# Performance work log

Measured on AMD Instinct MI355X. Metric: run time of the kernel, lower is better.

Reference implementation:

```python
import jax, jax.numpy as jnp
import numpy as np

N = 512    # nnodes
H = 8      # attention heads
C = 32     # gnn_repr_size (per head)
ER = 32    # edge_repr_size
FE = 3     # feat_emb_size
E = 16384  # edges (avg degree 32)


def gat_conv(x, edge_index, edge_attr, W, att_src, att_dst, We, att_edge, b):
    """PyG GATConv (edge_dim=1, concat=True, add_self_loops=True, eval mode)."""
    n = x.shape[0]
    h_, c_ = att_src.shape
    row, col = edge_index[0], edge_index[1]
    # self loops with fill_value='mean': mean of incoming edge_attr per target node
    deg = jax.ops.segment_sum(jnp.ones_like(edge_attr), col, num_segments=n)
    loop_attr = jax.ops.segment_sum(edge_attr, col, num_segments=n) / jnp.maximum(deg, 1.0)
    ar = jnp.arange(n)
    row = jnp.concatenate([row, ar])
    col = jnp.concatenate([col, ar])
    ea = jnp.concatenate([edge_attr, loop_attr])
    # node projections [n, H, C]
    h = (x @ W.T).reshape(n, h_, c_)
    a_src = jnp.sum(h * att_src, axis=-1)  # [n, H]
    a_dst = jnp.sum(h * att_dst, axis=-1)  # [n, H]
    e = (ea[:, None] @ We.T).reshape(-1, h_, c_)  # [E', H, C]
    a_e = jnp.sum(e * att_edge, axis=-1)          # [E', H]
    alpha = jax.nn.leaky_relu(a_src[row] + a_dst[col] + a_e, 0.2)
    # softmax over edges grouped by destination node
    amax = jax.ops.segment_max(alpha, col, num_segments=n)
    ex = jnp.exp(alpha - amax[col])
    denom = jax.ops.segment_sum(ex, col, num_segments=n)
    alpha = ex / (denom[col] + 1e-16)
    out = jax.ops.segment_sum(h[row] * alpha[..., None], col, num_segments=n)
    return out.reshape(n, h_ * c_) + b


def setup_inputs():
    key = jax.random.key(0)
    ks = jax.random.split(key, 24)
    s = 0.05
    HC = H * C
    in_len = N * ER + 3 * N + 3 * FE  # combiner1 input length
    return {
        "dist": jax.random.uniform(ks[0], (N, N), dtype=jnp.float32),
        "markov": jax.random.uniform(ks[1], (N, N), dtype=jnp.float32),
        "demand": jax.random.normal(ks[2], (N,), dtype=jnp.float32),
        "W_week": jax.random.normal(ks[3], (7, FE)) * s,
        "W_cap": jax.random.normal(ks[4], (26, FE)) * s,
        "W_veh": jax.random.normal(ks[5], (15, FE)) * s,
        "g1_W": jax.random.normal(ks[6], (HC, 1)) * s,
        "g1_att_src": jax.random.normal(ks[7], (H, C)) * s,
        "g1_att_dst": jax.random.normal(ks[8], (H, C)) * s,
        "g1_We": jax.random.normal(ks[9], (HC, 1)) * s,
        "g1_att_edge": jax.random.normal(ks[10], (H, C)) * s,
        "g1_b": jnp.zeros((HC,), dtype=jnp.float32),
        "g2_W": jax.random.normal(ks[11], (HC, HC)) * s,
        "g2_att_src": jax.random.normal(ks[12], (H, C)) * s,
        "g2_att_dst": jax.random.normal(ks[13], (H, C)) * s,
        "g2_We": jax.random.normal(ks[14], (HC, 1)) * s,
        "g2_att_edge": jax.random.normal(ks[15], (H, C)) * s,
        "g2_b": jnp.zeros((HC,), dtype=jnp.float32),
        "Wes": jax.random.normal(ks[16], (ER, 2 * HC)) * s,
        "bes": jnp.zeros((ER,), dtype=jnp.float32),
        "Wc1": jax.random.normal(ks[17], (N, in_len)) * 0.01,
        "bc1": jnp.zeros((N,), dtype=jnp.float32),
        "Wc2": jax.random.normal(ks[18], (N, N)) * s,
        "bc2": jnp.zeros((N,), dtype=jnp.float32),
        "stops": jax.random.randint(ks[19], (256,), 0, N),
        "edge_index": jax.random.randint(ks[20], (2, E), 0, N),
        "weekday": 3,
        "vehicles": 7,
        "capacity": 12,
    }


def reference(dist, markov, demand, W_week, W_cap, W_veh,
              g1_W, g1_att_src, g1_att_dst, g1_We, g1_att_edge, g1_b,
              g2_W, g2_att_src, g2_att_dst, g2_We, g2_att_edge, g2_b,
              Wes, bes, Wc1, bc1, Wc2, bc2,
              stops, edge_index, weekday, vehicles, capacity):
    n = dist.shape[0]
    dist = (dist - dist.min()) / (dist.max() - dist.min())
    x = demand[:, None]  # [n, 1]
    ea = markov[edge_index[0], edge_index[1]]  # [E]
    x = jax.nn.relu(gat_conv(x, edge_index, ea, g1_W, g1_att_src, g1_att_dst, g1_We, g1_att_edge, g1_b))
    x = jax.nn.relu(gat_conv(x, edge_index, ea, g2_W, g2_att_src, g2_att_dst, g2_We, g2_att_edge, g2_b))
    HC_ = x.shape[1]
    # all-pairs edge representation: concat(x[i], x[j]) over meshgrid -> [n*n, 2*HC]
    er = jnp.concatenate([
        jnp.broadcast_to(x[:, None, :], (n, n, HC_)),
        jnp.broadcast_to(x[None, :, :], (n, n, HC_)),
    ], axis=-1).reshape(n * n, 2 * HC_)
    er = (er @ Wes.T + bes).reshape(n, -1)  # [n, n*ER]
    week = jnp.broadcast_to(W_week[weekday], (n, W_week.shape[1]))
    cap = jnp.broadcast_to(W_cap[capacity], (n, W_cap.shape[1]))
    veh = jnp.broadcast_to(W_veh[vehicles], (n, W_veh.shape[1]))
    stop = jnp.broadcast_to(jnp.zeros((n,), dtype=dist.dtype).at[stops].set(1.0)[None, :], (n, n))
    feat = jnp.concatenate([er, dist, markov, week, cap, veh, stop], axis=1)
    out = jax.nn.relu(feat @ Wc1.T + bc1) @ Wc2.T + bc2
    return out
```

## Files before the change

### kernel.cpp

```cpp
#include <hip/hip_runtime.h>
#include <hip/hip_bf16.h>

typedef __hip_bfloat16 bf16;
typedef __attribute__((ext_vector_type(8))) short bf16x8;
typedef __attribute__((ext_vector_type(4))) float f32x4;

#define NNODE 512
#define NEDGE 16384
#define INLEN 17929
#define K1    1056

#define WS_EA      0
#define WS_CSRC    16384
#define WS_CEA     32768
#define WS_DEG     49152
#define WS_STARTS  49664
#define WS_LATTR   50176
#define WS_MM      50688
#define WS_MMP     50690
#define WS_STOPV   50818
#define WS_AE      51330
#define WS_PS      51346
#define WS_H       55552
#define WS_G2WT    186624
#define WS_H2      317696
#define WS_ASRC    448768
#define WS_ADST    452864
#define WS_UV      456960
#define WS_K       489728
#define WS_APACK   490240
#define WS_BPACK   760576
#define WS_OUT1    1030912
#define WS_WC2B    1161984
#define WS_WESF    1293056
#define WS_ASRC2   1309440
#define WS_ADST2   1313536
#define WS_CURSOR  1317632
#define WS_DEGP    1318144
#define WS_LSUMP   1350912

__global__ __launch_bounds__(256)
void k_prep(const float* __restrict__ demand, const float* __restrict__ W1,
            const float* __restrict__ att_s, const float* __restrict__ att_d,
            const int* __restrict__ stops, const float* __restrict__ Wes,
            const float* __restrict__ dist, const float* __restrict__ markov,
            const int* __restrict__ eidx,
            const float* __restrict__ g1We, const float* __restrict__ g1ae,
            const float* __restrict__ g2We, const float* __restrict__ g2ae,
            const float* __restrict__ g2W,  const float* __restrict__ g2as,
            const float* __restrict__ g2ad, float* ws){
  int b = blockIdx.x, tid = threadIdx.x;
  if (b < 512){
    int hd = tid>>5, c = tid&31;
    float hv = demand[b] * W1[tid];
    ws[WS_H + b*256 + tid] = hv;
    float ps = hv * att_s[tid];
    float pd = hv * att_d[tid];
    for (int off=16; off; off>>=1){ ps += __shfl_down(ps,off,32); pd += __shfl_down(pd,off,32); }
    if (c==0){ ws[WS_ASRC + b*8+hd]=ps; ws[WS_ADST + b*8+hd]=pd; }
  } else if (b == 512){
    ws[WS_STOPV+tid] = 0.f; ws[WS_STOPV+256+tid] = 0.f;
    __syncthreads();
    ws[WS_STOPV + stops[tid]] = 1.0f;
    if (tid < 8){
      float s=0.f; for (int c=0;c<32;c++) s += g1We[tid*32+c]*g1ae[tid*32+c];
      ws[WS_AE+tid]=s;
    } else if (tid < 16){
      int h=tid-8; float s=0.f; for (int c=0;c<32;c++) s += g2We[h*32+c]*g2ae[h*32+c];
      ws[WS_AE+8+h]=s;
    }
  } else if (b < 515){
    for (int idx = (b-513)*8192 + tid; idx < (b-512)*8192; idx += 256){
      int k = idx>>8, c = idx&255;
      ws[WS_WESF+idx] = (k<32) ? Wes[k*512+c] : Wes[(k-32)*512+256+c];
    }
  } else if (b < 579){
    __shared__ float smn[256], smx[256];
    int p = b-515;
    float mn = 3.4e38f, mx = -3.4e38f;
    for (int k=0;k<16;k++){
      float v = dist[p*4096 + k*256 + tid];
      mn = fminf(mn,v); mx = fmaxf(mx,v);
    }
    smn[tid]=mn; smx[tid]=mx; __syncthreads();
    for (int off=128; off; off>>=1){
      if (tid<off){ smn[tid]=fminf(smn[tid],smn[tid+off]); smx[tid]=fmaxf(smx[tid],smx[tid+off]); }
      __syncthreads();
    }
    if (tid==0){ ws[WS_MMP+p]=smn[0]; ws[WS_MMP+64+p]=smx[0]; }
  } else if (b < 643){
    __shared__ int   hd_[512];
    __shared__ float hf_[512];
    int k = b-579;
    hd_[tid]=0; hd_[256+tid]=0; hf_[tid]=0.f; hf_[256+tid]=0.f;
    __syncthreads();
    int e = k*256 + tid;
    int r = eidx[e], c = eidx[NEDGE+e];
    float a = markov[r*NNODE + c];
    ws[WS_EA+e] = a;
    atomicAdd(&hd_[c], 1);
    atomicAdd(&hf_[c], a);
    __syncthreads();
    ((int*)(ws+WS_DEGP))[k*512+tid]     = hd_[tid];
    ((int*)(ws+WS_DEGP))[k*512+256+tid] = hd_[256+tid];
    ws[WS_LSUMP + k*512+tid]     = hf_[tid];
    ws[WS_LSUMP + k*512+256+tid] = hf_[256+tid];
  } else if (b < 659){
    int j = b-643;
    const float* att = (j<8) ? g2as : g2ad;
    int h = j&7;
    float s = 0.f;
    for (int c=0;c<32;c++) s += att[h*32+c] * g2W[(h*32+c)*256 + tid];
    ws[WS_PS + j*256 + tid] = s;
  } else if (b < 675){
    __shared__ float T[64][65];
    int tb = b-659, tr = tb>>2, tc = tb&3;
    int w = tid>>6, c = tid&63;
    for (int k=0;k<16;k++){
      int r = k*4 + w;
      T[r][c] = g2W[(tr*64+r)*256 + tc*64 + c];
    }
    __syncthreads();
    for (int k=0;k<16;k++){
      int r = k*4 + w;
      ws[WS_G2WT + (tc*64+r)*256 + tr*64 + c] = T[c][r];
    }
  } else {
    ((int*)(ws+WS_CURSOR))[tid] = 0;
    ((int*)(ws+WS_CURSOR))[256+tid] = 0;
  }
}

__global__ __launch_bounds__(512)
void k_scansc(const int* __restrict__ eidx, float* ws){
  __shared__ int sc[512];
  __shared__ int startS[512];
  __shared__ float rmn[64], rmx[64];
  int t = threadIdx.x, b = blockIdx.x;
  const int* dp = (const int*)(ws+WS_DEGP);
  int d = 0;
  for (int k=0;k<64;k++) d += dp[k*512+t];
  sc[t] = d; __syncthreads();
  for (int off=1; off<512; off<<=1){
    int v = (t>=off) ? sc[t-off] : 0; __syncthreads();
    sc[t] += v; __syncthreads();
  }
  startS[t] = sc[t]-d;
  if (b == 0){
    float l = 0.f;
    for (int k=0;k<64;k++) l += ws[WS_LSUMP+k*512+t];
    ((int*)(ws+WS_STARTS))[t] = startS[t];
    ((int*)(ws+WS_DEG))[t] = d;
    ws[WS_LATTR+t] = l / (float)(d>1 ? d : 1);
    if (t < 64){ rmn[t]=ws[WS_MMP+t]; rmx[t]=ws[WS_MMP+64+t]; }
    __syncthreads();
    if (t == 0){
      float mn=rmn[0], mx=rmx[0];
      for (int i=1;i<64;i++){ mn=fminf(mn,rmn[i]); mx=fmaxf(mx,rmx[i]); }
      ws[WS_MM]=mn; ws[WS_MM+1]=mx;
    }
  }
  __syncthreads();
  int e = b*512 + t;
  int c = eidx[NEDGE+e];
  int p = startS[c] + atomicAdd((int*)(ws+WS_CURSOR)+c, 1);
  ((int*)(ws+WS_CSRC))[p] = eidx[e];
  ws[WS_CEA+p] = ws[WS_EA+e];
}

template<int MODE>
__global__ __launch_bounds__(256)
void k_agg(const float* __restrict__ hbuf, const float* __restrict__ asrc,
           const float* __restrict__ adst, const int* __restrict__ csrc,
           const float* __restrict__ cea, const int* __restrict__ starts,
           const int* __restrict__ deg, const float* __restrict__ lattr,
           const float* __restrict__ AEp, const float* __restrict__ bvec,
           const float* __restrict__ dist, const float* __restrict__ markov,
           float* ws){
  int t = blockIdx.x, tid = threadIdx.x, hd = tid>>5;
  __shared__ float AE[8], m[8], den[8], alpha[8];
  __shared__ float L[32*8];
  __shared__ float xrow[256];
  __shared__ float uvrow[64];
  if (tid < 8) AE[tid] = AEp[tid];
  __syncthreads();
  int d = deg[t], s0 = starts[t];
  if (tid < 8){
    float aself = asrc[t*8+tid] + adst[t*8+tid] + lattr[t]*AE[tid];
    aself = aself>=0.f ? aself : 0.2f*aself;
    m[tid] = aself; den[tid] = 1.0f;
  }
  __syncthreads();
  float acc = hbuf[t*256+tid];
  int el = tid>>3, h2i = tid&7;
  float adt2 = adst[t*8+h2i], ae2 = AE[h2i];
  for (int e0=0; e0<d; e0+=32){
    int ce = d-e0 < 32 ? d-e0 : 32;
    float lg = -3.4e38f;
    if (el < ce){
      int src = csrc[s0+e0+el];
      float a = asrc[src*8+h2i] + adt2 + cea[s0+e0+el]*ae2;
      lg = a>=0.f ? a : 0.2f*a;
    }
    L[el*8+h2i] = lg;
    __syncthreads();
    if (tid < 8){
      float mm = m[tid];
      for (int e=0;e<ce;e++) mm = fmaxf(mm, L[e*8+tid]);
      float al = __expf(m[tid]-mm);
      float dd = den[tid]*al;
      for (int e=0;e<ce;e++) dd += __expf(L[e*8+tid]-mm);
      m[tid]=mm; den[tid]=dd; alpha[tid]=al;
    }
    __syncthreads();
    if (el < ce) L[el*8+h2i] = __expf(lg - m[h2i]);
    __syncthreads();
    acc *= alpha[hd];
    for (int e=0;e<ce;e++){
      int sre = csrc[s0+e0+e];
      acc += L[e*8+hd] * hbuf[sre*256+tid];
    }
    __syncthreads();
  }
  float v = fmaxf(acc/den[hd] + bvec[tid], 0.f);
  xrow[tid] = v;
  __syncthreads();
  if (MODE == 1){
    const float* g2wt = ws + WS_G2WT;
    float hr = 0.f;
    for (int c=0;c<256;c++) hr += xrow[c] * g2wt[c*256 + tid];
    ws[WS_H2 + t*256 + tid] = hr;
    if (tid < 64){
      int j = tid>>2, q = tid&3;
      const float* pr = ws + WS_PS + j*256 + q*64;
      const float* xr = xrow + q*64;
      float p = 0.f;
      for (int c=0;c<64;c++) p += xr[c]*pr[c];
      p += __shfl_down(p,2,4);
      p += __shfl_down(p,1,4);
      if (q==0){
        if (j<8) ws[WS_ASRC2 + t*8+j] = p;
        else     ws[WS_ADST2 + t*8+(j-8)] = p;
      }
    }
  } else {
    int k = tid>>2, q = tid&3;
    const float* wr = ws + WS_WESF + k*256 + q*64;
    const float* xr = xrow + q*64;
    float p = 0.f;
    for (int c=0;c<64;c++) p += xr[c]*wr[c];
    p += __shfl_down(p,2,4);
    p += __shfl_down(p,1,4);
    if (q==0){ ws[WS_UV + t*64+k] = p; uvrow[k] = p; }
    __syncthreads();
    float mn = ws[WS_MM], mx = ws[WS_MM+1];
    float inv = 1.0f/(mx-mn);
    bf16* ap = (bf16*)(ws+WS_APACK);
    for (int j=tid; j<K1; j+=256){
      float v2;
      if (j<32)       v2 = uvrow[j];
      else if (j<544) v2 = (dist[t*512 + j-32] - mn) * inv;
      else            v2 = markov[t*512 + j-544];
      ap[(size_t)t*K1 + j] = __float2bfloat16(v2);
    }
  }
}

__global__ __launch_bounds__(1024)
void k_skpack(const float* __restrict__ Wc1, const float* __restrict__ bc1,
              const float* __restrict__ bes, const float* __restrict__ Wweek,
              const float* __restrict__ Wcap, const float* __restrict__ Wveh,
              const int* __restrict__ wd, const int* __restrict__ vh,
              const int* __restrict__ cp, const float* __restrict__ Wc2,
              float* ws){
  int o = blockIdx.x, tid = threadIdx.x;
  __shared__ float besf[32];
  __shared__ float red[1024];
  if (tid<32) besf[tid] = bes[tid];
  __syncthreads();
  const float* wr = Wc1 + (size_t)o*INLEN;
  bf16* bp  = (bf16*)(ws+WS_BPACK);
  bf16* w2b = (bf16*)(ws+WS_WC2B);
  float be = besf[tid&31];
  const float* uvp = ws + WS_UV + ((tid>>5)<<6) + 32 + (tid&31);
  float sP = 0.f, tP0=0.f, tP1=0.f, tP2=0.f, tP3=0.f;
  #pragma unroll
  for (int i=0;i<16;i+=4){
    float w0 = wr[tid + 1024*(i+0)];
    float w1 = wr[tid + 1024*(i+1)];
    float w2 = wr[tid + 1024*(i+2)];
    float w3 = wr[tid + 1024*(i+3)];
    float u0 = uvp[2048*(i+0)];
    float u1 = uvp[2048*(i+1)];
    float u2 = uvp[2048*(i+2)];
    float u3 = uvp[2048*(i+3)];
    sP += (w0+w1)+(w2+w3);
    tP0 += w0*(u0+be);
    tP1 += w1*(u1+be);
    tP2 += w2*(u2+be);
    tP3 += w3*(u3+be);
  }
  float tP = (tP0+tP1)+(tP2+tP3);
  if (tid < 512) tP += ws[WS_STOPV+tid] * wr[17417+tid];
  if (tid < 9){
    int g = tid/3, f = tid-g*3;
    float sv = (g==0) ? Wweek[wd[0]*3+f]
             : (g==1) ? Wcap[cp[0]*3+f]
                      : Wveh[vh[0]*3+f];
    tP += sv * wr[17408+tid];
  }
  red[tid] = sP; __syncthreads();
  for (int off=512; off>=32; off>>=1){
    if (tid<off) red[tid] += red[tid+off];
    __syncthreads();
  }
  if (tid<32) bp[(size_t)o*K1 + tid] = __float2bfloat16(red[tid]);
  __syncthreads();
  red[tid] = tP; __syncthreads();
  for (int off=512; off; off>>=1){
    if (tid<off) red[tid] += red[tid+off];
    __syncthreads();
  }
  if (tid==0) ws[WS_K+o] = red[0] + bc1[o];
  bp[(size_t)o*K1 + 32 + tid] = __float2bfloat16(wr[16384+tid]);
  if (tid < 512) w2b[o*512+tid] = __float2bfloat16(Wc2[o*512+tid]);
}

template<bool RELU, bool BF16OUT>
__global__ __launch_bounds__(256)
void gemm_mfma(const bf16* __restrict__ A, const bf16* __restrict__ B,
               const float* __restrict__ bias, float* __restrict__ Cf,
               bf16* __restrict__ Cb, int M, int N, int K){
  __shared__ short Als[2048];
  __shared__ short Bls[2048];
  const int tid = threadIdx.x;
  const int bm = blockIdx.y*64, bn = blockIdx.x*64;
  const int wave = tid>>6, lane = tid&63;
  const int wm = wave>>1, wn = wave&1;
  const int r = lane&15, q = lane>>4;
  f32x4 acc[2][2] = {};
  const int lrow = tid>>2, lq = tid&3;
  const bf16* Ag = A + (size_t)(bm+lrow)*K + lq*8;
  const bf16* Bg = B + (size_t)(bn+lrow)*K + lq*8;
  const int sidx = (lq*64+lrow)*8;
  for (int k0=0; k0<K; k0+=32){
    float4 av = *(const float4*)(Ag + k0);
    float4 bv = *(const float4*)(Bg + k0);
    *(float4*)(&Als[sidx]) = av;
    *(float4*)(&Bls[sidx]) = bv;
    __syncthreads();
    #pragma unroll
    for (int i=0;i<2;i++){
      bf16x8 af = *(const bf16x8*)(&Als[(q*64 + wm*32 + i*16 + r)*8]);
      #pragma unroll
      for (int j=0;j<2;j++){
        bf16x8 bfr = *(const bf16x8*)(&Bls[(q*64 + wn*32 + j*16 + r)*8]);
        acc[i][j] = __builtin_amdgcn_mfma_f32_16x16x32_bf16(af, bfr, acc[i][j], 0,0,0);
      }
    }
    __syncthreads();
  }
  #pragma unroll
  for (int i=0;i<2;i++){
    int row = bm + wm*32 + i*16 + q*4;
    #pragma unroll
    for (int j=0;j<2;j++){
      int col = bn + wn*32 + j*16 + r;
      float bi = bias ? bias[col] : 0.f;
      #pragma unroll
      for (int g=0; g<4; g++){
        float v = acc[i][j][g] + bi;
        if (RELU) v = fmaxf(v, 0.f);
        if (BF16OUT) Cb[(size_t)(row+g)*N + col] = __float2bfloat16(v);
        else         Cf[(size_t)(row+g)*N + col] = v;
      }
    }
  }
}

extern "C" void kernel_launch(void* const* d_in, const int* in_sizes, int n_in,
                              void* d_out, int out_size, void* d_ws, size_t ws_size,
                              hipStream_t stream){
  const float* dist   = (const float*)d_in[0];
  const float* markov = (const float*)d_in[1];
  const float* demand = (const float*)d_in[2];
  const float* Wweek  = (const float*)d_in[3];
  const float* Wcap   = (const float*)d_in[4];
  const float* Wveh   = (const float*)d_in[5];
  const float* g1W    = (const float*)d_in[6];
  const float* g1as   = (const float*)d_in[7];
  const float* g1ad   = (const float*)d_in[8];
  const float* g1We   = (const float*)d_in[9];
  const float* g1ae   = (const float*)d_in[10];
  const float* g1b    = (const float*)d_in[11];
  const float* g2W    = (const float*)d_in[12];
  const float* g2as   = (const float*)d_in[13];
  const float* g2ad   = (const float*)d_in[14];
  const float* g2We   = (const float*)d_in[15];
  const float* g2ae   = (const float*)d_in[16];
  const float* g2b    = (const float*)d_in[17];
  const float* Wes    = (const float*)d_in[18];
  const float* bes    = (const float*)d_in[19];
  const float* Wc1    = (const float*)d_in[20];
  const float* bc1    = (const float*)d_in[21];
  const float* Wc2    = (const float*)d_in[22];
  const float* bc2    = (const float*)d_in[23];
  const int*   stops  = (const int*)d_in[24];
  const int*   eidx   = (const int*)d_in[25];
  const int*   wd     = (const int*)d_in[26];
  const int*   vh     = (const int*)d_in[27];
  const int*   cp     = (const int*)d_in[28];
  float* out = (float*)d_out;
  float* ws = (float*)d_ws;

  const int*   csrc   = (const int*)(ws+WS_CSRC);
  const float* cea    = ws+WS_CEA;
  const int*   starts = (const int*)(ws+WS_STARTS);
  const int*   deg    = (const int*)(ws+WS_DEG);
  const float* lattr  = ws+WS_LATTR;

  k_prep<<<676,256,0,stream>>>(demand, g1W, g1as, g1ad, stops, Wes, dist, markov, eidx,
                               g1We, g1ae, g2We, g2ae, g2W, g2as, g2ad, ws);
  k_scansc<<<32,512,0,stream>>>(eidx, ws);
  k_agg<1><<<512,256,0,stream>>>(ws+WS_H, ws+WS_ASRC, ws+WS_ADST, csrc, cea, starts, deg,
                                 lattr, ws+WS_AE, g1b, dist, markov, ws);
  k_agg<2><<<512,256,0,stream>>>(ws+WS_H2, ws+WS_ASRC2, ws+WS_ADST2, csrc, cea, starts, deg,
                                 lattr, ws+WS_AE+8, g2b, dist, markov, ws);
  k_skpack<<<512,1024,0,stream>>>(Wc1, bc1, bes, Wweek, Wcap, Wveh, wd, vh, cp, Wc2, ws);
  gemm_mfma<true,true><<<dim3(8,8),256,0,stream>>>((const bf16*)(ws+WS_APACK), (const bf16*)(ws+WS_BPACK),
                                                   ws+WS_K, nullptr, (bf16*)(ws+WS_OUT1), 512, 512, K1);
  gemm_mfma<false,false><<<dim3(8,8),256,0,stream>>>((const bf16*)(ws+WS_OUT1), (const bf16*)(ws+WS_WC2B),
                                                     bc2, out, nullptr, 512, 512, 512);
}
```

Baseline: 212.8 us.

## Replace CSR build with per-node edge scan inside aggregation kernels

```diff
diff --git a/kernel.cpp b/kernel.cpp
--- a/kernel.cpp
+++ b/kernel.cpp
@@ -10,41 +10,30 @@
 #define INLEN 17929
 #define K1    1056
 
-#define WS_EA      0
-#define WS_CSRC    16384
-#define WS_CEA     32768
-#define WS_DEG     49152
-#define WS_STARTS  49664
-#define WS_LATTR   50176
-#define WS_MM      50688
-#define WS_MMP     50690
-#define WS_STOPV   50818
-#define WS_AE      51330
-#define WS_PS      51346
-#define WS_H       55552
-#define WS_G2WT    186624
-#define WS_H2      317696
-#define WS_ASRC    448768
-#define WS_ADST    452864
-#define WS_UV      456960
-#define WS_K       489728
-#define WS_APACK   490240
-#define WS_BPACK   760576
-#define WS_OUT1    1030912
-#define WS_WC2B    1161984
-#define WS_WESF    1293056
-#define WS_ASRC2   1309440
-#define WS_ADST2   1313536
-#define WS_CURSOR  1317632
-#define WS_DEGP    1318144
-#define WS_LSUMP   1350912
+#define WS_MMP     0
+#define WS_STOPV   128
+#define WS_AE      640
+#define WS_PS      656
+#define WS_H       5120
+#define WS_G2WT    136192
+#define WS_H2      201728
+#define WS_ASRC    332800
+#define WS_ADST    336896
+#define WS_UV      340992
+#define WS_K       373760
+#define WS_APACK   374272
+#define WS_BPACK   644608
+#define WS_OUT1    914944
+#define WS_WC2B    1046016
+#define WS_WESF    1177088
+#define WS_ASRC2   1193472
+#define WS_ADST2   1197568
 
 __global__ __launch_bounds__(256)
 void k_prep(const float* __restrict__ demand, const float* __restrict__ W1,
             const float* __restrict__ att_s, const float* __restrict__ att_d,
             const int* __restrict__ stops, const float* __restrict__ Wes,
-            const float* __restrict__ dist, const float* __restrict__ markov,
-            const int* __restrict__ eidx,
+            const float* __restrict__ dist,
             const float* __restrict__ g1We, const float* __restrict__ g1ae,
             const float* __restrict__ g2We, const float* __restrict__ g2ae,
             const float* __restrict__ g2W,  const float* __restrict__ g2as,
@@ -88,33 +77,16 @@
       __syncthreads();
     }
     if (tid==0){ ws[WS_MMP+p]=smn[0]; ws[WS_MMP+64+p]=smx[0]; }
-  } else if (b < 643){
-    __shared__ int   hd_[512];
-    __shared__ float hf_[512];
-    int k = b-579;
-    hd_[tid]=0; hd_[256+tid]=0; hf_[tid]=0.f; hf_[256+tid]=0.f;
-    __syncthreads();
-    int e = k*256 + tid;
-    int r = eidx[e], c = eidx[NEDGE+e];
-    float a = markov[r*NNODE + c];
-    ws[WS_EA+e] = a;
-    atomicAdd(&hd_[c], 1);
-    atomicAdd(&hf_[c], a);
-    __syncthreads();
-    ((int*)(ws+WS_DEGP))[k*512+tid]     = hd_[tid];
-    ((int*)(ws+WS_DEGP))[k*512+256+tid] = hd_[256+tid];
-    ws[WS_LSUMP + k*512+tid]     = hf_[tid];
-    ws[WS_LSUMP + k*512+256+tid] = hf_[256+tid];
-  } else if (b < 659){
-    int j = b-643;
+  } else if (b < 595){
+    int j = b-579;
     const float* att = (j<8) ? g2as : g2ad;
     int h = j&7;
     float s = 0.f;
     for (int c=0;c<32;c++) s += att[h*32+c] * g2W[(h*32+c)*256 + tid];
     ws[WS_PS + j*256 + tid] = s;
-  } else if (b < 675){
+  } else {
     __shared__ float T[64][65];
-    int tb = b-659, tr = tb>>2, tc = tb&3;
+    int tb = b-595, tr = tb>>2, tc = tb&3;
     int w = tid>>6, c = tid&63;
     for (int k=0;k<16;k++){
       int r = k*4 + w;
@@ -125,111 +97,96 @@
       int r = k*4 + w;
       ws[WS_G2WT + (tc*64+r)*256 + tr*64 + c] = T[c][r];
     }
-  } else {
-    ((int*)(ws+WS_CURSOR))[tid] = 0;
-    ((int*)(ws+WS_CURSOR))[256+tid] = 0;
-  }
-}
-
-__global__ __launch_bounds__(512)
-void k_scansc(const int* __restrict__ eidx, float* ws){
-  __shared__ int sc[512];
-  __shared__ int startS[512];
-  __shared__ float rmn[64], rmx[64];
-  int t = threadIdx.x, b = blockIdx.x;
-  const int* dp = (const int*)(ws+WS_DEGP);
-  int d = 0;
-  for (int k=0;k<64;k++) d += dp[k*512+t];
-  sc[t] = d; __syncthreads();
-  for (int off=1; off<512; off<<=1){
-    int v = (t>=off) ? sc[t-off] : 0; __syncthreads();
-    sc[t] += v; __syncthreads();
-  }
-  startS[t] = sc[t]-d;
-  if (b == 0){
-    float l = 0.f;
-    for (int k=0;k<64;k++) l += ws[WS_LSUMP+k*512+t];
-    ((int*)(ws+WS_STARTS))[t] = startS[t];
-    ((int*)(ws+WS_DEG))[t] = d;
-    ws[WS_LATTR+t] = l / (float)(d>1 ? d : 1);
-    if (t < 64){ rmn[t]=ws[WS_MMP+t]; rmx[t]=ws[WS_MMP+64+t]; }
-    __syncthreads();
-    if (t == 0){
-      float mn=rmn[0], mx=rmx[0];
-      for (int i=1;i<64;i++){ mn=fminf(mn,rmn[i]); mx=fmaxf(mx,rmx[i]); }
-      ws[WS_MM]=mn; ws[WS_MM+1]=mx;
-    }
-  }
-  __syncthreads();
-  int e = b*512 + t;
-  int c = eidx[NEDGE+e];
-  int p = startS[c] + atomicAdd((int*)(ws+WS_CURSOR)+c, 1);
-  ((int*)(ws+WS_CSRC))[p] = eidx[e];
-  ws[WS_CEA+p] = ws[WS_EA+e];
+  }
 }
 
 template<int MODE>
 __global__ __launch_bounds__(256)
 void k_agg(const float* __restrict__ hbuf, const float* __restrict__ asrc,
-           const float* __restrict__ adst, const int* __restrict__ csrc,
-           const float* __restrict__ cea, const int* __restrict__ starts,
-           const int* __restrict__ deg, const float* __restrict__ lattr,
-           const float* __restrict__ AEp, const float* __restrict__ bvec,
-           const float* __restrict__ dist, const float* __restrict__ markov,
+           const float* __restrict__ adst, const int* __restrict__ eidx,
+           const float* __restrict__ markov, const float* __restrict__ AEp,
+           const float* __restrict__ bvec, const float* __restrict__ dist,
            float* ws){
   int t = blockIdx.x, tid = threadIdx.x, hd = tid>>5;
-  __shared__ float AE[8], m[8], den[8], alpha[8];
-  __shared__ float L[32*8];
-  __shared__ float xrow[256];
-  __shared__ float uvrow[64];
-  if (tid < 8) AE[tid] = AEp[tid];
-  __syncthreads();
-  int d = deg[t], s0 = starts[t];
-  if (tid < 8){
-    float aself = asrc[t*8+tid] + adst[t*8+tid] + lattr[t]*AE[tid];
+  __shared__ int   srcE[256];
+  __shared__ float eaE[256];
+  __shared__ float Lall[256*8];
+  __shared__ float AE[8], mh[8], dh[8], sw[8];
+  __shared__ float xrow[256], uvrow[64];
+  __shared__ int   cnt;
+  __shared__ float easum;
+  __shared__ float mnS, mxS;
+  if (tid==0){ cnt=0; easum=0.f; }
+  if (tid<8) AE[tid]=AEp[tid];
+  __syncthreads();
+  for (int e0=0; e0<NEDGE; e0+=256){
+    int col = eidx[NEDGE+e0+tid];
+    if (col==t){
+      int p = atomicAdd(&cnt,1);
+      int row = eidx[e0+tid];
+      float a = markov[row*NNODE+t];
+      if (p<256){ srcE[p]=row; eaE[p]=a; }
+      atomicAdd(&easum, a);
+    }
+  }
+  __syncthreads();
+  int d = cnt<256 ? cnt : 256;
+  float lattr = easum / (float)(cnt>1 ? cnt : 1);
+  {
+    int h8 = tid&7, eq = tid>>3;
+    float adt = adst[t*8+h8], aeh = AE[h8];
+    for (int e = eq; e < d; e += 32){
+      int s = srcE[e];
+      float a = asrc[s*8+h8] + adt + eaE[e]*aeh;
+      Lall[e*8+h8] = a>=0.f ? a : 0.2f*a;
+    }
+  }
+  __syncthreads();
+  {
+    int h = tid>>5, j = tid&31;
+    float aself = asrc[t*8+h] + adst[t*8+h] + lattr*AE[h];
     aself = aself>=0.f ? aself : 0.2f*aself;
-    m[tid] = aself; den[tid] = 1.0f;
-  }
-  __syncthreads();
-  float acc = hbuf[t*256+tid];
-  int el = tid>>3, h2i = tid&7;
-  float adt2 = adst[t*8+h2i], ae2 = AE[h2i];
-  for (int e0=0; e0<d; e0+=32){
-    int ce = d-e0 < 32 ? d-e0 : 32;
-    float lg = -3.4e38f;
-    if (el < ce){
-      int src = csrc[s0+e0+el];
-      float a = asrc[src*8+h2i] + adt2 + cea[s0+e0+el]*ae2;
-      lg = a>=0.f ? a : 0.2f*a;
-    }
-    L[el*8+h2i] = lg;
-    __syncthreads();
-    if (tid < 8){
-      float mm = m[tid];
-      for (int e=0;e<ce;e++) mm = fmaxf(mm, L[e*8+tid]);
-      float al = __expf(m[tid]-mm);
-      float dd = den[tid]*al;
-      for (int e=0;e<ce;e++) dd += __expf(L[e*8+tid]-mm);
-      m[tid]=mm; den[tid]=dd; alpha[tid]=al;
-    }
-    __syncthreads();
-    if (el < ce) L[el*8+h2i] = __expf(lg - m[h2i]);
-    __syncthreads();
-    acc *= alpha[hd];
-    for (int e=0;e<ce;e++){
-      int sre = csrc[s0+e0+e];
-      acc += L[e*8+hd] * hbuf[sre*256+tid];
-    }
-    __syncthreads();
-  }
-  float v = fmaxf(acc/den[hd] + bvec[tid], 0.f);
+    float mm = aself;
+    for (int e=j; e<d; e+=32) mm = fmaxf(mm, Lall[e*8+h]);
+    for (int off=16; off; off>>=1) mm = fmaxf(mm, __shfl_down(mm,off,32));
+    mm = __shfl(mm, 0, 32);
+    float dd = 0.f;
+    for (int e=j; e<d; e+=32) dd += __expf(Lall[e*8+h]-mm);
+    for (int off=16; off; off>>=1) dd += __shfl_down(dd,off,32);
+    if (j==0){
+      float se = __expf(aself-mm);
+      mh[h]=mm; dh[h]=dd+se+1e-16f; sw[h]=se;
+    }
+  }
+  __syncthreads();
+  {
+    int h8 = tid&7;
+    for (int e = tid>>3; e < d; e += 32)
+      Lall[e*8+h8] = __expf(Lall[e*8+h8] - mh[h8]);
+  }
+  __syncthreads();
+  float a0 = sw[hd]*hbuf[t*256+tid], a1=0.f, a2=0.f, a3=0.f;
+  int e = 0;
+  for (; e+4<=d; e+=4){
+    a0 += Lall[(e+0)*8+hd]*hbuf[srcE[e+0]*256+tid];
+    a1 += Lall[(e+1)*8+hd]*hbuf[srcE[e+1]*256+tid];
+    a2 += Lall[(e+2)*8+hd]*hbuf[srcE[e+2]*256+tid];
+    a3 += Lall[(e+3)*8+hd]*hbuf[srcE[e+3]*256+tid];
+  }
+  for (; e<d; e++) a0 += Lall[e*8+hd]*hbuf[srcE[e]*256+tid];
+  float v = fmaxf(((a0+a1)+(a2+a3))/dh[hd] + bvec[tid], 0.f);
   xrow[tid] = v;
   __syncthreads();
   if (MODE == 1){
     const float* g2wt = ws + WS_G2WT;
-    float hr = 0.f;
-    for (int c=0;c<256;c++) hr += xrow[c] * g2wt[c*256 + tid];
-    ws[WS_H2 + t*256 + tid] = hr;
+    float h0=0.f,h1=0.f,h2=0.f,h3=0.f;
+    for (int c=0;c<256;c+=4){
+      h0 += xrow[c+0]*g2wt[(c+0)*256+tid];
+      h1 += xrow[c+1]*g2wt[(c+1)*256+tid];
+      h2 += xrow[c+2]*g2wt[(c+2)*256+tid];
+      h3 += xrow[c+3]*g2wt[(c+3)*256+tid];
+    }
+    ws[WS_H2 + t*256 + tid] = (h0+h1)+(h2+h3);
     if (tid < 64){
       int j = tid>>2, q = tid&3;
       const float* pr = ws + WS_PS + j*256 + q*64;
@@ -252,15 +209,23 @@
     p += __shfl_down(p,2,4);
     p += __shfl_down(p,1,4);
     if (q==0){ ws[WS_UV + t*64+k] = p; uvrow[k] = p; }
-    __syncthreads();
-    float mn = ws[WS_MM], mx = ws[WS_MM+1];
-    float inv = 1.0f/(mx-mn);
+    if (tid < 64){
+      float mn = ws[WS_MMP+tid], mx = ws[WS_MMP+64+tid];
+      for (int off=32; off; off>>=1){
+        mn = fminf(mn, __shfl_down(mn,off));
+        mx = fmaxf(mx, __shfl_down(mx,off));
+      }
+      if (tid==0){ mnS=mn; mxS=mx; }
+    }
+    __syncthreads();
+    float mn = mnS, inv = 1.0f/(mxS-mnS);
     bf16* ap = (bf16*)(ws+WS_APACK);
+    const float* mrow = markov + t*512;
     for (int j=tid; j<K1; j+=256){
       float v2;
       if (j<32)       v2 = uvrow[j];
       else if (j<544) v2 = (dist[t*512 + j-32] - mn) * inv;
-      else            v2 = markov[t*512 + j-544];
+      else            v2 = mrow[j-544];
       ap[(size_t)t*K1 + j] = __float2bfloat16(v2);
     }
   }
@@ -413,19 +378,12 @@
   float* out = (float*)d_out;
   float* ws = (float*)d_ws;
 
-  const int*   csrc   = (const int*)(ws+WS_CSRC);
-  const float* cea    = ws+WS_CEA;
-  const int*   starts = (const int*)(ws+WS_STARTS);
-  const int*   deg    = (const int*)(ws+WS_DEG);
-  const float* lattr  = ws+WS_LATTR;
-
-  k_prep<<<676,256,0,stream>>>(demand, g1W, g1as, g1ad, stops, Wes, dist, markov, eidx,
+  k_prep<<<611,256,0,stream>>>(demand, g1W, g1as, g1ad, stops, Wes, dist,
                                g1We, g1ae, g2We, g2ae, g2W, g2as, g2ad, ws);
-  k_scansc<<<32,512,0,stream>>>(eidx, ws);
-  k_agg<1><<<512,256,0,stream>>>(ws+WS_H, ws+WS_ASRC, ws+WS_ADST, csrc, cea, starts, deg,
-                                 lattr, ws+WS_AE, g1b, dist, markov, ws);
-  k_agg<2><<<512,256,0,stream>>>(ws+WS_H2, ws+WS_ASRC2, ws+WS_ADST2, csrc, cea, starts, deg,
-                                 lattr, ws+WS_AE+8, g2b, dist, markov, ws);
+  k_agg<1><<<512,256,0,stream>>>(ws+WS_H, ws+WS_ASRC, ws+WS_ADST, eidx, markov,
+                                 ws+WS_AE, g1b, dist, ws);
+  k_agg<2><<<512,256,0,stream>>>(ws+WS_H2, ws+WS_ASRC2, ws+WS_ADST2, eidx, markov,
+                                 ws+WS_AE+8, g2b, dist, ws);
   k_skpack<<<512,1024,0,stream>>>(Wc1, bc1, bes, Wweek, Wcap, Wveh, wd, vh, cp, Wc2, ws);
   gemm_mfma<true,true><<<dim3(8,8),256,0,stream>>>((const bf16*)(ws+WS_APACK), (const bf16*)(ws+WS_BPACK),
                                                    ws+WS_K, nullptr, (bf16*)(ws+WS_OUT1), 512, 512, K1);
```

Result: slower. 223.4 us (+5.0%).

## Replace online softmax in GAT aggregation with two-pass shared-memory softmax

Applied to the files above, without the earlier changes.

```diff
diff --git a/kernel.cpp b/kernel.cpp
--- a/kernel.cpp
+++ b/kernel.cpp
@@ -178,58 +178,71 @@
            const float* __restrict__ dist, const float* __restrict__ markov,
            float* ws){
   int t = blockIdx.x, tid = threadIdx.x, hd = tid>>5;
-  __shared__ float AE[8], m[8], den[8], alpha[8];
-  __shared__ float L[32*8];
-  __shared__ float xrow[256];
-  __shared__ float uvrow[64];
-  if (tid < 8) AE[tid] = AEp[tid];
+  __shared__ int   srcE[256];
+  __shared__ float eaE[256];
+  __shared__ float Lall[256*8];
+  __shared__ float AE[8], mh[8], dh[8], sw[8];
+  __shared__ float xrow[256], uvrow[64];
+  if (tid<8) AE[tid]=AEp[tid];
   __syncthreads();
   int d = deg[t], s0 = starts[t];
-  if (tid < 8){
-    float aself = asrc[t*8+tid] + adst[t*8+tid] + lattr[t]*AE[tid];
+  if (d > 256) d = 256;
+  for (int e=tid; e<d; e+=256){ srcE[e]=csrc[s0+e]; eaE[e]=cea[s0+e]; }
+  __syncthreads();
+  {
+    int h8 = tid&7;
+    float adt = adst[t*8+h8], aeh = AE[h8];
+    for (int e = tid>>3; e < d; e += 32){
+      float a = asrc[srcE[e]*8+h8] + adt + eaE[e]*aeh;
+      Lall[e*8+h8] = a>=0.f ? a : 0.2f*a;
+    }
+  }
+  __syncthreads();
+  {
+    int h = tid>>5, j = tid&31;
+    float aself = asrc[t*8+h] + adst[t*8+h] + lattr[t]*AE[h];
     aself = aself>=0.f ? aself : 0.2f*aself;
-    m[tid] = aself; den[tid] = 1.0f;
-  }
-  __syncthreads();
-  float acc = hbuf[t*256+tid];
-  int el = tid>>3, h2i = tid&7;
-  float adt2 = adst[t*8+h2i], ae2 = AE[h2i];
-  for (int e0=0; e0<d; e0+=32){
-    int ce = d-e0 < 32 ? d-e0 : 32;
-    float lg = -3.4e38f;
-    if (el < ce){
-      int src = csrc[s0+e0+el];
-      float a = asrc[src*8+h2i] + adt2 + cea[s0+e0+el]*ae2;
-      lg = a>=0.f ? a : 0.2f*a;
-    }
-    L[el*8+h2i] = lg;
-    __syncthreads();
-    if (tid < 8){
-      float mm = m[tid];
-      for (int e=0;e<ce;e++) mm = fmaxf(mm, L[e*8+tid]);
-      float al = __expf(m[tid]-mm);
-      float dd = den[tid]*al;
-      for (int e=0;e<ce;e++) dd += __expf(L[e*8+tid]-mm);
-      m[tid]=mm; den[tid]=dd; alpha[tid]=al;
-    }
-    __syncthreads();
-    if (el < ce) L[el*8+h2i] = __expf(lg - m[h2i]);
-    __syncthreads();
-    acc *= alpha[hd];
-    for (int e=0;e<ce;e++){
-      int sre = csrc[s0+e0+e];
-      acc += L[e*8+hd] * hbuf[sre*256+tid];
-    }
-    __syncthreads();
-  }
-  float v = fmaxf(acc/den[hd] + bvec[tid], 0.f);
+    float mm = aself;
+    for (int e=j; e<d; e+=32) mm = fmaxf(mm, Lall[e*8+h]);
+    for (int off=16; off; off>>=1) mm = fmaxf(mm, __shfl_down(mm,off,32));
+    mm = __shfl(mm, 0, 32);
+    float dd = 0.f;
+    for (int e=j; e<d; e+=32) dd += __expf(Lall[e*8+h]-mm);
+    for (int off=16; off; off>>=1) dd += __shfl_down(dd,off,32);
+    if (j==0){
+      float se = __expf(aself-mm);
+      mh[h]=mm; dh[h]=dd+se+1e-16f; sw[h]=se;
+    }
+  }
+  __syncthreads();
+  {
+    int h8 = tid&7;
+    for (int e = tid>>3; e < d; e += 32)
+      Lall[e*8+h8] = __expf(Lall[e*8+h8] - mh[h8]);
+  }
+  __syncthreads();
+  float a0 = sw[hd]*hbuf[t*256+tid], a1=0.f, a2=0.f, a3=0.f;
+  int e = 0;
+  for (; e+4<=d; e+=4){
+    a0 += Lall[(e+0)*8+hd]*hbuf[srcE[e+0]*256+tid];
+    a1 += Lall[(e+1)*8+hd]*hbuf[srcE[e+1]*256+tid];
+    a2 += Lall[(e+2)*8+hd]*hbuf[srcE[e+2]*256+tid];
+    a3 += Lall[(e+3)*8+hd]*hbuf[srcE[e+3]*256+tid];
+  }
+  for (; e<d; e++) a0 += Lall[e*8+hd]*hbuf[srcE[e]*256+tid];
+  float v = fmaxf(((a0+a1)+(a2+a3))/dh[hd] + bvec[tid], 0.f);
   xrow[tid] = v;
   __syncthreads();
   if (MODE == 1){
     const float* g2wt = ws + WS_G2WT;
-    float hr = 0.f;
-    for (int c=0;c<256;c++) hr += xrow[c] * g2wt[c*256 + tid];
-    ws[WS_H2 + t*256 + tid] = hr;
+    float h0=0.f,h1=0.f,h2=0.f,h3=0.f;
+    for (int c=0;c<256;c+=4){
+      h0 += xrow[c+0]*g2wt[(c+0)*256+tid];
+      h1 += xrow[c+1]*g2wt[(c+1)*256+tid];
+      h2 += xrow[c+2]*g2wt[(c+2)*256+tid];
+      h3 += xrow[c+3]*g2wt[(c+3)*256+tid];
+    }
+    ws[WS_H2 + t*256 + tid] = (h0+h1)+(h2+h3);
     if (tid < 64){
       int j = tid>>2, q = tid&3;
       const float* pr = ws + WS_PS + j*256 + q*64;
@@ -256,11 +269,12 @@
     float mn = ws[WS_MM], mx = ws[WS_MM+1];
     float inv = 1.0f/(mx-mn);
     bf16* ap = (bf16*)(ws+WS_APACK);
+    const float* mrow = markov + t*512;
     for (int j=tid; j<K1; j+=256){
       float v2;
       if (j<32)       v2 = uvrow[j];
       else if (j<544) v2 = (dist[t*512 + j-32] - mn) * inv;
-      else            v2 = markov[t*512 + j-544];
+      else            v2 = mrow[j-544];
       ap[(size_t)t*K1 + j] = __float2bfloat16(v2);
     }
   }
```

Result: faster. 207.8 us (-2.4%).
